# Performance work log

Measured on AMD Instinct MI355X. Metric: run time of the kernel, lower is better.

## Reference

```python
import jax, jax.numpy as jnp
import numpy as np


def _proj(x, w, b):
    # 1x1 conv as channel matmul: x (n,c,h,w), w (k,c), b (k,) -> (n,k,h,w)
    return jnp.einsum('nchw,kc->nkhw', x, w) + b[None, :, None, None]


def setup_inputs() -> dict:
    key = jax.random.key(0)
    ks = jax.random.split(key, 9)
    cin, cinter = 256, 128
    n, h, w = 4, 64, 64
    s = lambda fan_in: 1.0 / np.sqrt(fan_in)
    return {
        'x': jax.random.normal(ks[0], (n, cin, h, w), jnp.float32),
        'theta_w': jax.random.normal(ks[1], (cinter, cin), jnp.float32) * s(cin),
        'theta_b': jax.random.normal(ks[2], (cinter,), jnp.float32) * 0.01,
        'phi_w': jax.random.normal(ks[3], (cinter, cin), jnp.float32) * s(cin),
        'phi_b': jax.random.normal(ks[4], (cinter,), jnp.float32) * 0.01,
        'g_w': jax.random.normal(ks[5], (cinter, cin), jnp.float32) * s(cin),
        'g_b': jax.random.normal(ks[6], (cinter,), jnp.float32) * 0.01,
        'w_w': jax.random.normal(ks[7], (cin, cinter), jnp.float32) * s(cinter),
        'w_b': jax.random.normal(ks[8], (cin,), jnp.float32) * 0.01,
    }


def reference(x, theta_w, theta_b, phi_w, phi_b, g_w, g_b, w_w, w_b):
    n, c, h, w = x.shape
    cinter = theta_w.shape[0]
    hw = h * w
    theta_x = _proj(x, theta_w, theta_b).reshape(n, cinter, hw)  # (n,ci,HW)
    phi_x = _proj(x, phi_w, phi_b).reshape(n, cinter, hw)        # (n,ci,HW)
    g_x = _proj(x, g_w, g_b).reshape(n, cinter, hw)              # (n,ci,HW)
    # f_x = phi^T @ theta : (n, HW, HW), softmax over last dim (theta positions)
    f_x = jnp.einsum('nci,ncj->nij', phi_x, theta_x)
    f_x = jax.nn.softmax(f_x, axis=-1)
    # attended = g @ f : (n, ci, HW)
    att = jnp.einsum('nci,nij->ncj', g_x, f_x).reshape(n, cinter, h, w)
    res_x = _proj(att, w_w, w_b)  # (n, c, h, w)
    return x + res_x
```

## Files before the change

### kernel.cpp

```cpp
#include <hip/hip_runtime.h>
#include <hip/hip_bf16.h>

#define B_ 4
#define C_ 256
#define CI_ 128
#define P_ 4096
#define LOG2E 1.44269504088896340736f

typedef __attribute__((ext_vector_type(8))) _Float16 half8;
typedef __attribute__((ext_vector_type(8))) short short8;
typedef __attribute__((ext_vector_type(4))) short short4v;
typedef __attribute__((ext_vector_type(4))) float floatx4;

__device__ __forceinline__ float bf2f(ushort h) {
  union { unsigned u; float f; } v; v.u = ((unsigned)h) << 16; return v.f;
}
__device__ __forceinline__ ushort f2bf(float f) {
  union { float f; unsigned u; } v; v.f = f;
  unsigned r = v.u + 0x7FFFu + ((v.u >> 16) & 1u);
  return (ushort)(r >> 16);
}
__device__ __forceinline__ ushort f2h(float f) {
  _Float16 h = (_Float16)f;
  union { _Float16 h; ushort u; } v; v.h = h; return v.u;
}

#define MFMA16(a, b, c) __builtin_amdgcn_mfma_f32_16x16x32_f16((a), (b), (c), 0, 0, 0)

__device__ __forceinline__ int detect_bf16(const ushort* __restrict__ xu) {
  __shared__ int cnt_;
  if (threadIdx.x == 0) cnt_ = 0;
  __syncthreads();
  int local = 0;
  int t = threadIdx.x & 255;
#pragma unroll
  for (int s = 0; s < 8; ++s) {
    ushort u = xu[(t * 8 + s) * 2];
    int e = (u >> 7) & 0xFF;
    local += (e >= 0x70 && e <= 0x84) ? 1 : 0;
  }
  atomicAdd(&cnt_, local);
  __syncthreads();
  return cnt_ > 1024;
}

__global__ void k_cvtwb(const void* __restrict__ s0, const void* __restrict__ s1,
                        const void* __restrict__ s2, const void* __restrict__ s3,
                        const void* __restrict__ tb, const void* __restrict__ pb,
                        const void* __restrict__ gb, const void* __restrict__ wb,
                        const ushort* __restrict__ xu,
                        ushort* __restrict__ dstW, float* __restrict__ biasf) {
  int is_bf16 = detect_bf16(xu);
  const void* srcs[4] = {s0, s1, s2, s3};
  int a = blockIdx.y;
  int bx = blockIdx.x;
  int t = threadIdx.x;
  if (bx < 128) {
    int i = bx * 256 + t;
    float v = is_bf16 ? bf2f(((const ushort*)srcs[a])[i]) : ((const float*)srcs[a])[i];
    dstW[a * 32768 + i] = f2h(v);
  } else {
    if (a < 3) {
      const void* bs = (a == 0) ? tb : (a == 1) ? pb : gb;
      if (t < 128) {
        float v = is_bf16 ? bf2f(((const ushort*)bs)[t]) : ((const float*)bs)[t];
        biasf[a * 128 + t] = v;
      }
    } else {
      float v = is_bf16 ? bf2f(((const ushort*)wb)[t]) : ((const float*)wb)[t];
      biasf[384 + t] = v;
    }
  }
}

__global__ void k_transpose(const void* __restrict__ xv, ushort* __restrict__ xT) {
  int is_bf16 = detect_bf16((const ushort*)xv);
  __shared__ __align__(16) ushort tile[64][72];
  int b = blockIdx.z;
  int cb = blockIdx.y * 64;
  int pb = blockIdx.x * 64;
  int t = threadIdx.x;
#pragma unroll
  for (int it = 0; it < 2; ++it) {
    int lin = it * 256 + t;
    int c = lin >> 3;
    int p = (lin & 7) * 8;
    size_t base = ((size_t)(b * C_) + cb + c) * P_ + pb + p;
    float vv[8];
    if (is_bf16) {
      short8 v = *(const short8*)((const ushort*)xv + base);
#pragma unroll
      for (int i = 0; i < 8; ++i) vv[i] = bf2f((ushort)v[i]);
    } else {
      const float* xf = (const float*)xv;
      float4 v0 = *(const float4*)(xf + base);
      float4 v1 = *(const float4*)(xf + base + 4);
      vv[0] = v0.x; vv[1] = v0.y; vv[2] = v0.z; vv[3] = v0.w;
      vv[4] = v1.x; vv[5] = v1.y; vv[6] = v1.z; vv[7] = v1.w;
    }
#pragma unroll
    for (int i = 0; i < 8; ++i) {
      int iw = (i + t) & 7;
      tile[p + iw][c] = f2h(vv[iw]);
    }
  }
  __syncthreads();
#pragma unroll
  for (int it = 0; it < 2; ++it) {
    int lin = it * 256 + t;
    int p = lin >> 3;
    int c = (lin & 7) * 8;
    short8 v = *(const short8*)&tile[p][c];
    *(short8*)(xT + ((size_t)(b * P_) + pb + p) * C_ + cb + c) = v;
  }
}

__global__ __launch_bounds__(256, 4) void k_proj(
    const ushort* __restrict__ xT, const ushort* __restrict__ Wh,
    const float* __restrict__ biasf,
    ushort* __restrict__ thetaT, ushort* __restrict__ phiT,
    ushort* __restrict__ g) {
  int t = threadIdx.x;
  int w = t >> 6, lane = t & 63, l = lane & 15, q = lane >> 4;
  int pblk = blockIdx.x * 32;
  int b = blockIdx.y;
  floatx4 acc[2][6];
#pragma unroll
  for (int ps = 0; ps < 2; ++ps)
#pragma unroll
    for (int ks = 0; ks < 6; ++ks) acc[ps][ks] = (floatx4){0.f, 0.f, 0.f, 0.f};
  const ushort* xrow[2];
#pragma unroll
  for (int ps = 0; ps < 2; ++ps)
    xrow[ps] = xT + ((size_t)(b * P_) + pblk + ps * 16 + l) * C_;
  const ushort* wrow[6];
  int prj[6], kloc[6];
#pragma unroll
  for (int ks = 0; ks < 6; ++ks) {
    int kg = w * 96 + ks * 16;
    prj[ks] = kg >> 7;
    kloc[ks] = kg & 127;
    wrow[ks] = Wh + prj[ks] * 32768 + (size_t)(kloc[ks] + l) * C_;
  }
  for (int c = 0; c < C_; c += 32) {
    half8 av[2], wv[6];
#pragma unroll
    for (int ps = 0; ps < 2; ++ps) av[ps] = *(const half8*)(xrow[ps] + c + q * 8);
#pragma unroll
    for (int ks = 0; ks < 6; ++ks) wv[ks] = *(const half8*)(wrow[ks] + c + q * 8);
#pragma unroll
    for (int ps = 0; ps < 2; ++ps)
#pragma unroll
      for (int ks = 0; ks < 6; ++ks)
        acc[ps][ks] = MFMA16(av[ps], wv[ks], acc[ps][ks]);
  }
#pragma unroll
  for (int ks = 0; ks < 6; ++ks) {
    float bias = biasf[prj[ks] * 128 + kloc[ks] + l];
#pragma unroll
    for (int ps = 0; ps < 2; ++ps) {
      floatx4 d = acc[ps][ks];
      if (prj[ks] < 2) {
        ushort* dst = (prj[ks] == 0 ? thetaT : phiT) +
                      ((size_t)(b * P_) + pblk + ps * 16 + q * 4) * CI_ + kloc[ks] + l;
#pragma unroll
        for (int r = 0; r < 4; ++r) dst[(size_t)r * CI_] = f2h(d[r] + bias);
      } else {
        ushort* dst = g + ((size_t)(b * CI_) + kloc[ks] + l) * P_ + pblk + ps * 16 + q * 4;
        short4v pk;
#pragma unroll
        for (int r = 0; r < 4; ++r) pk[r] = (short)f2h(d[r] + bias);
        *(short4v*)dst = pk;
      }
    }
  }
}

__global__ __launch_bounds__(256, 2) void k_stats(
    const ushort* __restrict__ phiT, const ushort* __restrict__ thetaT,
    float* __restrict__ part) {
  int t = threadIdx.x, w = t >> 6, lane = t & 63, l = lane & 15, q = lane >> 4;
  int i0 = blockIdx.x * 256, j0 = blockIdx.y * 512, b = blockIdx.z;
  half8 av[4][4];
#pragma unroll
  for (int is = 0; is < 4; ++is) {
    const ushort* pr = phiT + ((size_t)(b * P_) + i0 + w * 64 + is * 16 + l) * CI_;
#pragma unroll
    for (int ks = 0; ks < 4; ++ks) av[is][ks] = *(const half8*)(pr + ks * 32 + q * 8);
  }
  float sum[4][4];
#pragma unroll
  for (int is = 0; is < 4; ++is)
#pragma unroll
    for (int r = 0; r < 4; ++r) sum[is][r] = 0.f;
  const ushort* tb0 = thetaT + (size_t)b * P_ * CI_;
  for (int jc = 0; jc < 16; ++jc) {
    int j = j0 + jc * 32;
    half8 bv[2][4];
#pragma unroll
    for (int js = 0; js < 2; ++js) {
      const ushort* tr = tb0 + (size_t)(j + js * 16 + l) * CI_;
#pragma unroll
      for (int ks = 0; ks < 4; ++ks) bv[js][ks] = *(const half8*)(tr + ks * 32 + q * 8);
    }
    floatx4 accS[4][2];
#pragma unroll
    for (int is = 0; is < 4; ++is)
#pragma unroll
      for (int js = 0; js < 2; ++js) accS[is][js] = (floatx4){0.f, 0.f, 0.f, 0.f};
#pragma unroll
    for (int ks = 0; ks < 4; ++ks)
#pragma unroll
      for (int is = 0; is < 4; ++is)
#pragma unroll
        for (int js = 0; js < 2; ++js)
          accS[is][js] = MFMA16(av[is][ks], bv[js][ks], accS[is][js]);
#pragma unroll
    for (int is = 0; is < 4; ++is)
#pragma unroll
      for (int js = 0; js < 2; ++js)
#pragma unroll
        for (int r = 0; r < 4; ++r)
          sum[is][r] += exp2f(fmaf(accS[is][js][r], LOG2E, -64.f));
  }
#pragma unroll
  for (int d = 1; d < 16; d <<= 1)
#pragma unroll
    for (int is = 0; is < 4; ++is)
#pragma unroll
      for (int r = 0; r < 4; ++r) sum[is][r] += __shfl_xor(sum[is][r], d, 64);
  if (l == 0) {
#pragma unroll
    for (int is = 0; is < 4; ++is)
#pragma unroll
      for (int r = 0; r < 4; ++r)
        part[((size_t)blockIdx.y * B_ + b) * P_ + i0 + w * 64 + is * 16 + q * 4 + r] =
            sum[is][r];
  }
}

__global__ void k_lse(const float* __restrict__ part, float* __restrict__ o2) {
  int idx = blockIdx.x * 256 + threadIdx.x;
  float s = 0.f;
#pragma unroll
  for (int p = 0; p < 8; ++p) s += part[(size_t)p * (B_ * P_) + idx];
  o2[idx] = log2f(s) + 64.f;
}

__global__ __launch_bounds__(256, 1) void k_attn(
    const ushort* __restrict__ phiT, const ushort* __restrict__ thetaT,
    const ushort* __restrict__ g, const float* __restrict__ o2,
    ushort* __restrict__ attP) {
  __shared__ __align__(16) ushort thL[128][136];
  __shared__ __align__(16) ushort eL[128][136];
  int t = threadIdx.x;
  int w = t >> 6, lane = t & 63, l = lane & 15, q = lane >> 4;
  int j0 = blockIdx.x * 128, ih = blockIdx.y, b = blockIdx.z;
#pragma unroll
  for (int it = 0; it < 8; ++it) {
    int lin = it * 256 + t, row = lin >> 4, cg = (lin & 15) * 8;
    *(short8*)&thL[row][cg] =
        *(const short8*)(thetaT + ((size_t)(b * P_) + j0 + row) * CI_ + cg);
  }
  floatx4 accA[2][8];
#pragma unroll
  for (int cs = 0; cs < 2; ++cs)
#pragma unroll
    for (int js = 0; js < 8; ++js) accA[cs][js] = (floatx4){0.f, 0.f, 0.f, 0.f};
  __syncthreads();
  const float* orow = o2 + b * P_;
  half8 af[2][4];
  float ov[2][4];
  {
    int ibase = ih * 2048;
#pragma unroll
    for (int is = 0; is < 2; ++is) {
      int iG = ibase + w * 32 + is * 16;
      const ushort* pr = phiT + ((size_t)(b * P_) + iG + l) * CI_;
#pragma unroll
      for (int ks = 0; ks < 4; ++ks) af[is][ks] = *(const half8*)(pr + ks * 32 + q * 8);
#pragma unroll
      for (int r = 0; r < 4; ++r) ov[is][r] = orow[iG + q * 4 + r];
    }
  }
  for (int ic = 0; ic < 16; ++ic) {
    int ibase = ih * 2048 + ic * 128;
    half8 gf[2][4];
#pragma unroll
    for (int cs = 0; cs < 2; ++cs) {
      const ushort* gr = g + ((size_t)(b * CI_) + w * 32 + cs * 16 + l) * P_ + ibase;
#pragma unroll
      for (int ks = 0; ks < 4; ++ks) gf[cs][ks] = *(const half8*)(gr + ks * 32 + q * 8);
    }
    floatx4 accS[2][8];
#pragma unroll
    for (int is = 0; is < 2; ++is)
#pragma unroll
      for (int js = 0; js < 8; ++js) accS[is][js] = (floatx4){0.f, 0.f, 0.f, 0.f};
#pragma unroll
    for (int ks = 0; ks < 4; ++ks) {
      half8 bf[8];
#pragma unroll
      for (int js = 0; js < 8; ++js) bf[js] = *(const half8*)&thL[js * 16 + l][ks * 32 + q * 8];
#pragma unroll
      for (int is = 0; is < 2; ++is)
#pragma unroll
        for (int js = 0; js < 8; ++js) accS[is][js] = MFMA16(af[is][ks], bf[js], accS[is][js]);
    }
    ushort ev[2][8][4];
#pragma unroll
    for (int is = 0; is < 2; ++is)
#pragma unroll
      for (int js = 0; js < 8; ++js)
#pragma unroll
        for (int r = 0; r < 4; ++r) {
          float earg = fminf(fmaf(accS[is][js][r], LOG2E, -ov[is][r]), 0.5f);
          ev[is][js][r] = f2h(exp2f(earg));
        }
    __syncthreads();
#pragma unroll
    for (int is = 0; is < 2; ++is)
#pragma unroll
      for (int js = 0; js < 8; ++js) {
        short4v pk;
#pragma unroll
        for (int r = 0; r < 4; ++r) pk[r] = (short)ev[is][js][r];
        *(short4v*)&eL[js * 16 + l][w * 32 + is * 16 + q * 4] = pk;
      }
    __syncthreads();
    if (ic < 15) {
      int nb = ih * 2048 + (ic + 1) * 128;
#pragma unroll
      for (int is = 0; is < 2; ++is) {
        int iG = nb + w * 32 + is * 16;
        const ushort* pr = phiT + ((size_t)(b * P_) + iG + l) * CI_;
#pragma unroll
        for (int ks = 0; ks < 4; ++ks) af[is][ks] = *(const half8*)(pr + ks * 32 + q * 8);
#pragma unroll
        for (int r = 0; r < 4; ++r) ov[is][r] = orow[iG + q * 4 + r];
      }
    }
#pragma unroll
    for (int ks = 0; ks < 4; ++ks) {
      half8 ef[8];
#pragma unroll
      for (int js = 0; js < 8; ++js) ef[js] = *(const half8*)&eL[js * 16 + l][ks * 32 + q * 8];
#pragma unroll
      for (int cs = 0; cs < 2; ++cs)
#pragma unroll
        for (int js = 0; js < 8; ++js) accA[cs][js] = MFMA16(gf[cs][ks], ef[js], accA[cs][js]);
    }
  }
  ushort* ap = attP + (size_t)ih * (B_ * P_ * CI_);
#pragma unroll
  for (int cs = 0; cs < 2; ++cs)
#pragma unroll
    for (int js = 0; js < 8; ++js) {
      short4v pk;
#pragma unroll
      for (int r = 0; r < 4; ++r) pk[r] = (short)f2h(accA[cs][js][r]);
      *(short4v*)(ap + ((size_t)(b * P_) + j0 + js * 16 + l) * CI_ +
                  w * 32 + cs * 16 + q * 4) = pk;
    }
}

__global__ __launch_bounds__(256, 4) void k_out(
    const ushort* __restrict__ attP, const ushort* __restrict__ wwh,
    const float* __restrict__ biasf, const void* __restrict__ xv,
    void* __restrict__ outv) {
  int is_bf16 = detect_bf16((const ushort*)xv);
  int t = threadIdx.x;
  int w = t >> 6, lane = t & 63, l = lane & 15, q = lane >> 4;
  int p0 = blockIdx.x * 32, b = blockIdx.y;
  const ushort* a0 = attP + ((size_t)(b * P_) + p0) * CI_;
  const ushort* a1 = a0 + (size_t)(B_ * P_) * CI_;
  floatx4 accR[4][2];
#pragma unroll
  for (int kk = 0; kk < 4; ++kk)
#pragma unroll
    for (int js = 0; js < 2; ++js) accR[kk][js] = (floatx4){0.f, 0.f, 0.f, 0.f};
#pragma unroll
  for (int ks = 0; ks < 4; ++ks) {
    half8 wf[4], af[2];
#pragma unroll
    for (int kk = 0; kk < 4; ++kk)
      wf[kk] = *(const half8*)(wwh + (size_t)(w * 64 + kk * 16 + l) * CI_ + ks * 32 + q * 8);
#pragma unroll
    for (int js = 0; js < 2; ++js) {
      size_t off = (size_t)(js * 16 + l) * CI_ + ks * 32 + q * 8;
      half8 v0 = *(const half8*)(a0 + off);
      half8 v1 = *(const half8*)(a1 + off);
      af[js] = v0 + v1;
    }
#pragma unroll
    for (int kk = 0; kk < 4; ++kk)
#pragma unroll
      for (int js = 0; js < 2; ++js) accR[kk][js] = MFMA16(wf[kk], af[js], accR[kk][js]);
  }
#pragma unroll
  for (int kk = 0; kk < 4; ++kk)
#pragma unroll
    for (int r = 0; r < 4; ++r) {
      int c = w * 64 + kk * 16 + q * 4 + r;
      float bias = biasf[384 + c];
#pragma unroll
      for (int js = 0; js < 2; ++js) {
        int p = p0 + js * 16 + l;
        size_t idx = ((size_t)(b * C_) + c) * P_ + p;
        float val = accR[kk][js][r] + bias;
        if (is_bf16) {
          ((ushort*)outv)[idx] = f2bf(bf2f(((const ushort*)xv)[idx]) + val);
        } else {
          ((float*)outv)[idx] = ((const float*)xv)[idx] + val;
        }
      }
    }
}

extern "C" void kernel_launch(void* const* d_in, const int* in_sizes, int n_in,
                              void* d_out, int out_size, void* d_ws, size_t ws_size,
                              hipStream_t stream) {
  const void* x  = d_in[0];
  const void* tw = d_in[1];
  const void* tb = d_in[2];
  const void* pw = d_in[3];
  const void* pb = d_in[4];
  const void* gw = d_in[5];
  const void* gb = d_in[6];
  const void* ww = d_in[7];
  const void* wb = d_in[8];
  char* ws = (char*)d_ws;
  ushort* xT     = (ushort*)(ws);
  ushort* attP   = (ushort*)(ws);
  ushort* thetaT = (ushort*)(ws + (8u << 20));
  ushort* phiT   = (ushort*)(ws + (12u << 20));
  ushort* gbuf   = (ushort*)(ws + (16u << 20));
  float*  o2     = (float*)(ws + (20u << 20));
  float*  part   = (float*)(ws + (20u << 20) + (64u << 10));
  ushort* Wh     = (ushort*)(ws + (20u << 20) + (576u << 10));
  float*  biasf  = (float*)(ws + (20u << 20) + (832u << 10));

  k_cvtwb<<<dim3(129, 4), 256, 0, stream>>>(tw, pw, gw, ww, tb, pb, gb, wb,
                                            (const ushort*)x, Wh, biasf);
  k_transpose<<<dim3(64, 4, 4), 256, 0, stream>>>(x, xT);
  k_proj<<<dim3(128, 4), 256, 0, stream>>>(xT, Wh, biasf, thetaT, phiT, gbuf);
  k_stats<<<dim3(16, 8, 4), 256, 0, stream>>>(phiT, thetaT, part);
  k_lse<<<64, 256, 0, stream>>>(part, o2);
  k_attn<<<dim3(32, 2, 4), 256, 0, stream>>>(phiT, thetaT, gbuf, o2, attP);
  k_out<<<dim3(128, 4), 256, 0, stream>>>(attP, Wh + 3 * 32768, biasf, x, d_out);
}
```

Baseline: 238.1 us.

## Split attention over four key chunks, fuse prep kernels, pack fp16 conversions

Merges the weight/bias conversion and the x transpose into a single launch. When the workspace is large enough, the attention kernel splits the key dimension into four partial chunks instead of two, giving 512 blocks rather than 256, and raises the launch bound to two blocks per CU. The output kernel sums four partial buffers in that case. The exp/convert path now uses packed round-toward-zero fp16 conversion and drops the clamp on the exponent argument. The trade is more partial-sum traffic and reduced fp16 rounding precision, in return for better occupancy and load balance in the dominant attention kernel.

New measurement: 235.0 us. About the same (-1.3%).

```diff
diff --git a/kernel.cpp b/kernel.cpp
--- a/kernel.cpp
+++ b/kernel.cpp
@@ -8,6 +8,7 @@
 #define LOG2E 1.44269504088896340736f
 
 typedef __attribute__((ext_vector_type(8))) _Float16 half8;
+typedef __attribute__((ext_vector_type(2))) __fp16 fp16x2;
 typedef __attribute__((ext_vector_type(8))) short short8;
 typedef __attribute__((ext_vector_type(4))) short short4v;
 typedef __attribute__((ext_vector_type(4))) float floatx4;
@@ -23,6 +24,12 @@
 __device__ __forceinline__ ushort f2h(float f) {
   _Float16 h = (_Float16)f;
   union { _Float16 h; ushort u; } v; v.h = h; return v.u;
+}
+__device__ __forceinline__ uint2 pk4h(float a, float b, float c, float d) {
+  union { fp16x2 h[2]; uint2 u; } pk;
+  pk.h[0] = __builtin_amdgcn_cvt_pkrtz(a, b);
+  pk.h[1] = __builtin_amdgcn_cvt_pkrtz(c, d);
+  return pk.u;
 }
 
 #define MFMA16(a, b, c) __builtin_amdgcn_mfma_f32_16x16x32_f16((a), (b), (c), 0, 0, 0)
@@ -44,74 +51,71 @@
   return cnt_ > 1024;
 }
 
-__global__ void k_cvtwb(const void* __restrict__ s0, const void* __restrict__ s1,
-                        const void* __restrict__ s2, const void* __restrict__ s3,
-                        const void* __restrict__ tb, const void* __restrict__ pb,
-                        const void* __restrict__ gb, const void* __restrict__ wb,
-                        const ushort* __restrict__ xu,
-                        ushort* __restrict__ dstW, float* __restrict__ biasf) {
-  int is_bf16 = detect_bf16(xu);
-  const void* srcs[4] = {s0, s1, s2, s3};
-  int a = blockIdx.y;
-  int bx = blockIdx.x;
+__global__ void k_trc(const void* __restrict__ xv, ushort* __restrict__ xT,
+                      const void* __restrict__ s0, const void* __restrict__ s1,
+                      const void* __restrict__ s2, const void* __restrict__ s3,
+                      const void* __restrict__ tbv, const void* __restrict__ pbv,
+                      const void* __restrict__ gbv, const void* __restrict__ wbv,
+                      ushort* __restrict__ dstW, float* __restrict__ biasf) {
+  int is_bf16 = detect_bf16((const ushort*)xv);
+  int bid = blockIdx.x;
   int t = threadIdx.x;
-  if (bx < 128) {
-    int i = bx * 256 + t;
+  if (bid < 1024) {
+    __shared__ __align__(16) ushort tile[64][72];
+    int pb = (bid & 63) * 64;
+    int cb = ((bid >> 6) & 3) * 64;
+    int b = bid >> 8;
+#pragma unroll
+    for (int it = 0; it < 2; ++it) {
+      int lin = it * 256 + t;
+      int c = lin >> 3;
+      int p = (lin & 7) * 8;
+      size_t base = ((size_t)(b * C_) + cb + c) * P_ + pb + p;
+      float vv[8];
+      if (is_bf16) {
+        short8 v = *(const short8*)((const ushort*)xv + base);
+#pragma unroll
+        for (int i = 0; i < 8; ++i) vv[i] = bf2f((ushort)v[i]);
+      } else {
+        const float* xf = (const float*)xv;
+        float4 v0 = *(const float4*)(xf + base);
+        float4 v1 = *(const float4*)(xf + base + 4);
+        vv[0] = v0.x; vv[1] = v0.y; vv[2] = v0.z; vv[3] = v0.w;
+        vv[4] = v1.x; vv[5] = v1.y; vv[6] = v1.z; vv[7] = v1.w;
+      }
+#pragma unroll
+      for (int i = 0; i < 8; ++i) {
+        int iw = (i + t) & 7;
+        tile[p + iw][c] = f2h(vv[iw]);
+      }
+    }
+    __syncthreads();
+#pragma unroll
+    for (int it = 0; it < 2; ++it) {
+      int lin = it * 256 + t;
+      int p = lin >> 3;
+      int c = (lin & 7) * 8;
+      short8 v = *(const short8*)&tile[p][c];
+      *(short8*)(xT + ((size_t)(b * P_) + pb + p) * C_ + cb + c) = v;
+    }
+  } else if (bid < 1536) {
+    int wid = bid - 1024;
+    int a = wid >> 7;
+    const void* srcs[4] = {s0, s1, s2, s3};
+    int i = (wid & 127) * 256 + t;
     float v = is_bf16 ? bf2f(((const ushort*)srcs[a])[i]) : ((const float*)srcs[a])[i];
     dstW[a * 32768 + i] = f2h(v);
   } else {
-    if (a < 3) {
-      const void* bs = (a == 0) ? tb : (a == 1) ? pb : gb;
-      if (t < 128) {
-        float v = is_bf16 ? bf2f(((const ushort*)bs)[t]) : ((const float*)bs)[t];
-        biasf[a * 128 + t] = v;
-      }
-    } else {
-      float v = is_bf16 ? bf2f(((const ushort*)wb)[t]) : ((const float*)wb)[t];
-      biasf[384 + t] = v;
-    }
-  }
-}
-
-__global__ void k_transpose(const void* __restrict__ xv, ushort* __restrict__ xT) {
-  int is_bf16 = detect_bf16((const ushort*)xv);
-  __shared__ __align__(16) ushort tile[64][72];
-  int b = blockIdx.z;
-  int cb = blockIdx.y * 64;
-  int pb = blockIdx.x * 64;
-  int t = threadIdx.x;
-#pragma unroll
-  for (int it = 0; it < 2; ++it) {
-    int lin = it * 256 + t;
-    int c = lin >> 3;
-    int p = (lin & 7) * 8;
-    size_t base = ((size_t)(b * C_) + cb + c) * P_ + pb + p;
-    float vv[8];
-    if (is_bf16) {
-      short8 v = *(const short8*)((const ushort*)xv + base);
-#pragma unroll
-      for (int i = 0; i < 8; ++i) vv[i] = bf2f((ushort)v[i]);
-    } else {
-      const float* xf = (const float*)xv;
-      float4 v0 = *(const float4*)(xf + base);
-      float4 v1 = *(const float4*)(xf + base + 4);
-      vv[0] = v0.x; vv[1] = v0.y; vv[2] = v0.z; vv[3] = v0.w;
-      vv[4] = v1.x; vv[5] = v1.y; vv[6] = v1.z; vv[7] = v1.w;
-    }
-#pragma unroll
-    for (int i = 0; i < 8; ++i) {
-      int iw = (i + t) & 7;
-      tile[p + iw][c] = f2h(vv[iw]);
-    }
-  }
-  __syncthreads();
-#pragma unroll
-  for (int it = 0; it < 2; ++it) {
-    int lin = it * 256 + t;
-    int p = lin >> 3;
-    int c = (lin & 7) * 8;
-    short8 v = *(const short8*)&tile[p][c];
-    *(short8*)(xT + ((size_t)(b * P_) + pb + p) * C_ + cb + c) = v;
+    int idx = (bid - 1536) * 256 + t;
+    if (idx < 640) {
+      const void* src; int loc;
+      if (idx < 128)      { src = tbv; loc = idx; }
+      else if (idx < 256) { src = pbv; loc = idx - 128; }
+      else if (idx < 384) { src = gbv; loc = idx - 256; }
+      else                { src = wbv; loc = idx - 384; }
+      float v = is_bf16 ? bf2f(((const ushort*)src)[loc]) : ((const float*)src)[loc];
+      biasf[idx] = v;
+    }
   }
 }
 
@@ -247,10 +251,10 @@
   o2[idx] = log2f(s) + 64.f;
 }
 
-__global__ __launch_bounds__(256, 1) void k_attn(
+__global__ __launch_bounds__(256, 2) void k_attn(
     const ushort* __restrict__ phiT, const ushort* __restrict__ thetaT,
     const ushort* __restrict__ g, const float* __restrict__ o2,
-    ushort* __restrict__ attP) {
+    ushort* __restrict__ attPA, ushort* __restrict__ attPB, int nChunk) {
   __shared__ __align__(16) ushort thL[128][136];
   __shared__ __align__(16) ushort eL[128][136];
   int t = threadIdx.x;
@@ -269,22 +273,20 @@
     for (int js = 0; js < 8; ++js) accA[cs][js] = (floatx4){0.f, 0.f, 0.f, 0.f};
   __syncthreads();
   const float* orow = o2 + b * P_;
+  int istart = ih * nChunk * 128;
   half8 af[2][4];
   float ov[2][4];
-  {
-    int ibase = ih * 2048;
-#pragma unroll
-    for (int is = 0; is < 2; ++is) {
-      int iG = ibase + w * 32 + is * 16;
-      const ushort* pr = phiT + ((size_t)(b * P_) + iG + l) * CI_;
-#pragma unroll
-      for (int ks = 0; ks < 4; ++ks) af[is][ks] = *(const half8*)(pr + ks * 32 + q * 8);
-#pragma unroll
-      for (int r = 0; r < 4; ++r) ov[is][r] = orow[iG + q * 4 + r];
-    }
-  }
-  for (int ic = 0; ic < 16; ++ic) {
-    int ibase = ih * 2048 + ic * 128;
+#pragma unroll
+  for (int is = 0; is < 2; ++is) {
+    int iG = istart + w * 32 + is * 16;
+    const ushort* pr = phiT + ((size_t)(b * P_) + iG + l) * CI_;
+#pragma unroll
+    for (int ks = 0; ks < 4; ++ks) af[is][ks] = *(const half8*)(pr + ks * 32 + q * 8);
+#pragma unroll
+    for (int r = 0; r < 4; ++r) ov[is][r] = orow[iG + q * 4 + r];
+  }
+  for (int ic = 0; ic < nChunk; ++ic) {
+    int ibase = istart + ic * 128;
     half8 gf[2][4];
 #pragma unroll
     for (int cs = 0; cs < 2; ++cs) {
@@ -307,29 +309,26 @@
 #pragma unroll
         for (int js = 0; js < 8; ++js) accS[is][js] = MFMA16(af[is][ks], bf[js], accS[is][js]);
     }
-    ushort ev[2][8][4];
+    uint2 ep[2][8];
 #pragma unroll
     for (int is = 0; is < 2; ++is)
 #pragma unroll
+      for (int js = 0; js < 8; ++js) {
+        float e0 = exp2f(fmaf(accS[is][js][0], LOG2E, -ov[is][0]));
+        float e1 = exp2f(fmaf(accS[is][js][1], LOG2E, -ov[is][1]));
+        float e2 = exp2f(fmaf(accS[is][js][2], LOG2E, -ov[is][2]));
+        float e3 = exp2f(fmaf(accS[is][js][3], LOG2E, -ov[is][3]));
+        ep[is][js] = pk4h(e0, e1, e2, e3);
+      }
+    __syncthreads();
+#pragma unroll
+    for (int is = 0; is < 2; ++is)
+#pragma unroll
       for (int js = 0; js < 8; ++js)
-#pragma unroll
-        for (int r = 0; r < 4; ++r) {
-          float earg = fminf(fmaf(accS[is][js][r], LOG2E, -ov[is][r]), 0.5f);
-          ev[is][js][r] = f2h(exp2f(earg));
-        }
+        *(uint2*)&eL[js * 16 + l][w * 32 + is * 16 + q * 4] = ep[is][js];
     __syncthreads();
-#pragma unroll
-    for (int is = 0; is < 2; ++is)
-#pragma unroll
-      for (int js = 0; js < 8; ++js) {
-        short4v pk;
-#pragma unroll
-        for (int r = 0; r < 4; ++r) pk[r] = (short)ev[is][js][r];
-        *(short4v*)&eL[js * 16 + l][w * 32 + is * 16 + q * 4] = pk;
-      }
-    __syncthreads();
-    if (ic < 15) {
-      int nb = ih * 2048 + (ic + 1) * 128;
+    if (ic < nChunk - 1) {
+      int nb = istart + (ic + 1) * 128;
 #pragma unroll
       for (int is = 0; is < 2; ++is) {
         int iG = nb + w * 32 + is * 16;
@@ -351,29 +350,25 @@
         for (int js = 0; js < 8; ++js) accA[cs][js] = MFMA16(gf[cs][ks], ef[js], accA[cs][js]);
     }
   }
-  ushort* ap = attP + (size_t)ih * (B_ * P_ * CI_);
+  ushort* ap = (ih < 2 ? attPA : attPB) + (size_t)(ih & 1) * (B_ * P_ * CI_);
 #pragma unroll
   for (int cs = 0; cs < 2; ++cs)
 #pragma unroll
     for (int js = 0; js < 8; ++js) {
-      short4v pk;
-#pragma unroll
-      for (int r = 0; r < 4; ++r) pk[r] = (short)f2h(accA[cs][js][r]);
-      *(short4v*)(ap + ((size_t)(b * P_) + j0 + js * 16 + l) * CI_ +
-                  w * 32 + cs * 16 + q * 4) = pk;
+      uint2 pk = pk4h(accA[cs][js][0], accA[cs][js][1], accA[cs][js][2], accA[cs][js][3]);
+      *(uint2*)(ap + ((size_t)(b * P_) + j0 + js * 16 + l) * CI_ +
+                w * 32 + cs * 16 + q * 4) = pk;
     }
 }
 
 __global__ __launch_bounds__(256, 4) void k_out(
-    const ushort* __restrict__ attP, const ushort* __restrict__ wwh,
-    const float* __restrict__ biasf, const void* __restrict__ xv,
-    void* __restrict__ outv) {
+    const ushort* __restrict__ attPA, const ushort* __restrict__ attPB, int nIH,
+    const ushort* __restrict__ wwh, const float* __restrict__ biasf,
+    const void* __restrict__ xv, void* __restrict__ outv) {
   int is_bf16 = detect_bf16((const ushort*)xv);
   int t = threadIdx.x;
   int w = t >> 6, lane = t & 63, l = lane & 15, q = lane >> 4;
   int p0 = blockIdx.x * 32, b = blockIdx.y;
-  const ushort* a0 = attP + ((size_t)(b * P_) + p0) * CI_;
-  const ushort* a1 = a0 + (size_t)(B_ * P_) * CI_;
   floatx4 accR[4][2];
 #pragma unroll
   for (int kk = 0; kk < 4; ++kk)
@@ -387,10 +382,14 @@
       wf[kk] = *(const half8*)(wwh + (size_t)(w * 64 + kk * 16 + l) * CI_ + ks * 32 + q * 8);
 #pragma unroll
     for (int js = 0; js < 2; ++js) {
-      size_t off = (size_t)(js * 16 + l) * CI_ + ks * 32 + q * 8;
-      half8 v0 = *(const half8*)(a0 + off);
-      half8 v1 = *(const half8*)(a1 + off);
-      af[js] = v0 + v1;
+      size_t off = ((size_t)(b * P_) + p0 + js * 16 + l) * CI_ + ks * 32 + q * 8;
+      half8 s = *(const half8*)(attPA + off);
+      s = s + *(const half8*)(attPA + (size_t)(B_ * P_) * CI_ + off);
+      if (nIH == 4) {
+        s = s + *(const half8*)(attPB + off);
+        s = s + *(const half8*)(attPB + (size_t)(B_ * P_) * CI_ + off);
+      }
+      af[js] = s;
     }
 #pragma unroll
     for (int kk = 0; kk < 4; ++kk)
@@ -430,22 +429,27 @@
   const void* ww = d_in[7];
   const void* wb = d_in[8];
   char* ws = (char*)d_ws;
-  ushort* xT     = (ushort*)(ws);
-  ushort* attP   = (ushort*)(ws);
-  ushort* thetaT = (ushort*)(ws + (8u << 20));
-  ushort* phiT   = (ushort*)(ws + (12u << 20));
-  ushort* gbuf   = (ushort*)(ws + (16u << 20));
-  float*  o2     = (float*)(ws + (20u << 20));
-  float*  part   = (float*)(ws + (20u << 20) + (64u << 10));
-  ushort* Wh     = (ushort*)(ws + (20u << 20) + (576u << 10));
-  float*  biasf  = (float*)(ws + (20u << 20) + (832u << 10));
-
-  k_cvtwb<<<dim3(129, 4), 256, 0, stream>>>(tw, pw, gw, ww, tb, pb, gb, wb,
-                                            (const ushort*)x, Wh, biasf);
-  k_transpose<<<dim3(64, 4, 4), 256, 0, stream>>>(x, xT);
+  float*  o2     = (float*)(ws);
+  float*  part   = (float*)(ws + (64u << 10));
+  ushort* Wh     = (ushort*)(ws + (576u << 10));
+  float*  biasf  = (float*)(ws + (832u << 10));
+  ushort* xT     = (ushort*)(ws + (1u << 20));
+  ushort* attPA  = xT;
+  ushort* thetaT = (ushort*)(ws + (9u << 20));
+  ushort* phiT   = (ushort*)(ws + (13u << 20));
+  ushort* gbuf   = (ushort*)(ws + (17u << 20));
+  ushort* attPB  = (ushort*)(ws + (21u << 20));
+  int big = (ws_size >= (30u << 20)) ? 1 : 0;
+
+  k_trc<<<1539, 256, 0, stream>>>(x, xT, tw, pw, gw, ww, tb, pb, gb, wb, Wh, biasf);
   k_proj<<<dim3(128, 4), 256, 0, stream>>>(xT, Wh, biasf, thetaT, phiT, gbuf);
   k_stats<<<dim3(16, 8, 4), 256, 0, stream>>>(phiT, thetaT, part);
   k_lse<<<64, 256, 0, stream>>>(part, o2);
-  k_attn<<<dim3(32, 2, 4), 256, 0, stream>>>(phiT, thetaT, gbuf, o2, attP);
-  k_out<<<dim3(128, 4), 256, 0, stream>>>(attP, Wh + 3 * 32768, biasf, x, d_out);
-}
+  if (big) {
+    k_attn<<<dim3(32, 4, 4), 256, 0, stream>>>(phiT, thetaT, gbuf, o2, attPA, attPB, 8);
+    k_out<<<dim3(128, 4), 256, 0, stream>>>(attPA, attPB, 4, Wh + 3 * 32768, biasf, x, d_out);
+  } else {
+    k_attn<<<dim3(32, 2, 4), 256, 0, stream>>>(phiT, thetaT, gbuf, o2, attPA, attPB, 16);
+    k_out<<<dim3(128, 4), 256, 0, stream>>>(attPA, attPB, 2, Wh + 3 * 32768, biasf, x, d_out);
+  }
+}
```
